# Optimization experiments

Measured on AMD Instinct MI355X. Metric: run time of the kernel, lower is better.

Reference implementation:

```python
import jax, jax.numpy as jnp
import numpy as np

B, TQ, TK, QD, KD = 16, 256, 256, 512, 512

def setup_inputs() -> dict:
    key = jax.random.key(0)
    k = jax.random.split(key, 8)
    query = jax.random.normal(k[0], (B, TQ, QD), dtype=jnp.float32)
    keys = jax.random.normal(k[1], (B, TK, KD), dtype=jnp.float32)
    # linear_q: query_size -> key_size (stored as [in, out] for x @ W)
    Wq = jax.random.normal(k[2], (QD, KD), dtype=jnp.float32) * 0.02
    bq = jnp.zeros((KD,), dtype=jnp.float32)
    # linear_att: key_size -> 1
    w_att = jax.random.normal(k[3], (KD,), dtype=jnp.float32) * 0.02
    b_att = jnp.zeros((), dtype=jnp.float32)
    # linear_out: (query_size + key_size) -> query_size
    Wout = jax.random.normal(k[4], (QD + KD, QD), dtype=jnp.float32) * 0.02
    bout = jnp.zeros((QD,), dtype=jnp.float32)
    return {"query": query, "keys": keys, "Wq": Wq, "bq": bq,
            "w_att": w_att, "b_att": b_att, "Wout": Wout, "bout": bout}

def reference(query, keys, Wq, bq, w_att, b_att, Wout, bout):
    # att_query = linear_q(query): [b, t_q, n]
    att_query = query @ Wq + bq
    # Bahdanau additive score: tanh(q_i + k_j) . w + b  -> [b, t_q, t_k]
    sum_qk = jnp.tanh(att_query[:, :, None, :] + keys[:, None, :, :])  # b,tq,tk,n
    scores = jnp.einsum('bqkn,n->bqk', sum_qk, w_att) + b_att
    p = jax.nn.softmax(scores, axis=-1)  # softmax over t_k
    # values defaults to keys
    context = jnp.einsum('bqk,bkn->bqn', p, keys)
    # output transform: tanh(linear_out([query; context]))
    context = jnp.tanh(jnp.concatenate([query, context], axis=-1) @ Wout + bout)
    return context, p
```

## Files before the change

### kernel.cpp

```cpp
#include <hip/hip_runtime.h>


#define C2 2.88539008177792681f

typedef unsigned short u16;
typedef short s16x8 __attribute__((ext_vector_type(8)));
typedef float f32x4 __attribute__((ext_vector_type(4)));

__device__ __forceinline__ float fast_rcp(float x) { return __builtin_amdgcn_rcpf(x); }

__device__ __forceinline__ u16 f2bf(float f) {
  union { float f; unsigned u; } v; v.f = f;
  unsigned r = v.u + 0x7fffu + ((v.u >> 16) & 1u);
  return (u16)(r >> 16);
}
__device__ __forceinline__ unsigned packbf(float a, float b) {
  return (unsigned)f2bf(a) | ((unsigned)f2bf(b) << 16);
}

__global__ __launch_bounds__(256) void prep_kernel(
    const float* __restrict__ keys, float* __restrict__ Ek,
    const float* __restrict__ query, u16* __restrict__ qbf,
    const float* __restrict__ w_att, const float* __restrict__ b_att,
    float* __restrict__ Cout)
{
  __shared__ float red[4];
  const int t = threadIdx.x;
  const int bx = blockIdx.x;
  if (bx < 2048) {
    const size_t i4 = (size_t)bx * 256 + t;
    float4 v = ((const float4*)keys)[i4];
    float4 o;
    o.x = exp2f(C2 * v.x); o.y = exp2f(C2 * v.y);
    o.z = exp2f(C2 * v.z); o.w = exp2f(C2 * v.w);
    ((float4*)Ek)[i4] = o;
    if (bx == 0) {
      float wsum = w_att[t] + w_att[t + 256];
#pragma unroll
      for (int m = 32; m; m >>= 1) wsum += __shfl_xor(wsum, m);
      if ((t & 63) == 0) red[t >> 6] = wsum;
      __syncthreads();
      if (t == 0) Cout[0] = red[0] + red[1] + red[2] + red[3] + b_att[0];
    }
  } else {
    const size_t i8 = ((size_t)(bx - 2048) * 256 + t) * 8;
    float4 a = *(const float4*)&query[i8];
    float4 b = *(const float4*)&query[i8 + 4];
    unsigned p0 = packbf(a.x, a.y), p1 = packbf(a.z, a.w);
    unsigned p2 = packbf(b.x, b.y), p3 = packbf(b.z, b.w);
    *(int4*)&qbf[i8] = make_int4(p0, p1, p2, p3);
  }
}

__global__ __launch_bounds__(256) void transpose_w_bf16(
    const float* __restrict__ Wq, u16* __restrict__ Wqt,
    const float* __restrict__ Wout, u16* __restrict__ Woutt)
{
  __shared__ u16 tile[32][40];
  const int t = threadIdx.x;
  const int by = blockIdx.y;
  const float* W; u16* Wt; int K, k0;
  if (by < 16) { W = Wq;   Wt = Wqt;   K = 512;  k0 = by * 32; }
  else         { W = Wout; Wt = Woutt; K = 1024; k0 = (by - 16) * 32; }
  const int n0 = blockIdx.x * 32;
  const int r = t >> 3, c = (t & 7) * 4;
  float4 v = *(const float4*)&W[(size_t)(k0 + r) * 512 + n0 + c];
  tile[c + 0][r] = f2bf(v.x); tile[c + 1][r] = f2bf(v.y);
  tile[c + 2][r] = f2bf(v.z); tile[c + 3][r] = f2bf(v.w);
  __syncthreads();
  if (t < 128) {
    const int row = t >> 2, ch = (t & 3) * 8;
    unsigned p0 = (unsigned)tile[row][ch + 0] | ((unsigned)tile[row][ch + 1] << 16);
    unsigned p1 = (unsigned)tile[row][ch + 2] | ((unsigned)tile[row][ch + 3] << 16);
    unsigned p2 = (unsigned)tile[row][ch + 4] | ((unsigned)tile[row][ch + 5] << 16);
    unsigned p3 = (unsigned)tile[row][ch + 6] | ((unsigned)tile[row][ch + 7] << 16);
    *(int4*)&Wt[(size_t)(n0 + row) * K + k0 + ch] = make_int4(p0, p1, p2, p3);
  }
}

__global__ __launch_bounds__(256) void transpose_keys_bf16(
    const float* __restrict__ keys, u16* __restrict__ kbfT)
{
  __shared__ u16 tile[32][40];
  const int t = threadIdx.x;
  const int n0 = blockIdx.x * 32, k0 = blockIdx.y * 32, b = blockIdx.z;
  const float* src = keys + (size_t)b * 131072;
  u16* dst = kbfT + (size_t)b * 131072;
  const int r = t >> 3, c = (t & 7) * 4;
  float4 v = *(const float4*)&src[(size_t)(k0 + r) * 512 + n0 + c];
  tile[c + 0][r] = f2bf(v.x); tile[c + 1][r] = f2bf(v.y);
  tile[c + 2][r] = f2bf(v.z); tile[c + 3][r] = f2bf(v.w);
  __syncthreads();
  if (t < 128) {
    const int row = t >> 2, ch = (t & 3) * 8;
    unsigned p0 = (unsigned)tile[row][ch + 0] | ((unsigned)tile[row][ch + 1] << 16);
    unsigned p1 = (unsigned)tile[row][ch + 2] | ((unsigned)tile[row][ch + 3] << 16);
    unsigned p2 = (unsigned)tile[row][ch + 4] | ((unsigned)tile[row][ch + 5] << 16);
    unsigned p3 = (unsigned)tile[row][ch + 6] | ((unsigned)tile[row][ch + 7] << 16);
    *(int4*)&dst[(size_t)(n0 + row) * 256 + k0 + ch] = make_int4(p0, p1, p2, p3);
  }
}

__global__ __launch_bounds__(256) void gemm_mfma_bf16(
    const u16* __restrict__ A0, const u16* __restrict__ A1, int kSplit,
    const u16* __restrict__ Bt, const float* __restrict__ bias,
    float* __restrict__ C, int K, int act)
{
  __shared__ u16 As[64 * 72];
  __shared__ u16 Bs[64 * 72];
  const int t = threadIdx.x;
  const int lane = t & 63, wid = t >> 6;
  const int wm = wid >> 1, wn = wid & 1;
  const int col0 = blockIdx.x * 64, row0 = blockIdx.y * 64;
  const int lr = t >> 2, lc = (t & 3) * 16;
  const int fr = lane & 15, fg = (lane >> 4) * 8;

  f32x4 acc[2][2] = {};
  const int nIter = K >> 6;

  int4 a0v, a1v, b0v, b1v;
  {
    const u16* Asrc = (0 < kSplit) ? A0 : A1;
    a0v = *(const int4*)&Asrc[(size_t)(row0 + lr) * 512 + lc];
    a1v = *(const int4*)&Asrc[(size_t)(row0 + lr) * 512 + lc + 8];
    b0v = *(const int4*)&Bt[(size_t)(col0 + lr) * K + lc];
    b1v = *(const int4*)&Bt[(size_t)(col0 + lr) * K + lc + 8];
  }
  for (int it = 0; it < nIter; ++it) {
    __syncthreads();
    *(int4*)&As[lr * 72 + lc]     = a0v;
    *(int4*)&As[lr * 72 + lc + 8] = a1v;
    *(int4*)&Bs[lr * 72 + lc]     = b0v;
    *(int4*)&Bs[lr * 72 + lc + 8] = b1v;
    __syncthreads();

    if (it + 1 < nIter) {
      const int k0 = (it + 1) << 6;
      const u16* Asrc; int kc;
      if (k0 < kSplit) { Asrc = A0; kc = k0; } else { Asrc = A1; kc = k0 - kSplit; }
      a0v = *(const int4*)&Asrc[(size_t)(row0 + lr) * 512 + kc + lc];
      a1v = *(const int4*)&Asrc[(size_t)(row0 + lr) * 512 + kc + lc + 8];
      b0v = *(const int4*)&Bt[(size_t)(col0 + lr) * K + k0 + lc];
      b1v = *(const int4*)&Bt[(size_t)(col0 + lr) * K + k0 + lc + 8];
    }

#pragma unroll
    for (int ks = 0; ks < 2; ++ks) {
      s16x8 af[2], bf[2];
#pragma unroll
      for (int m = 0; m < 2; ++m)
        af[m] = *(const s16x8*)&As[(wm * 32 + m * 16 + fr) * 72 + ks * 32 + fg];
#pragma unroll
      for (int n = 0; n < 2; ++n)
        bf[n] = *(const s16x8*)&Bs[(wn * 32 + n * 16 + fr) * 72 + ks * 32 + fg];
#pragma unroll
      for (int m = 0; m < 2; ++m)
#pragma unroll
        for (int n = 0; n < 2; ++n)
          acc[m][n] = __builtin_amdgcn_mfma_f32_16x16x32_bf16(af[m], bf[n], acc[m][n], 0, 0, 0);
    }
  }

  const int fq = lane >> 4;
#pragma unroll
  for (int n = 0; n < 2; ++n) {
    const int col = col0 + wn * 32 + n * 16 + fr;
    const float bv = bias[col];
#pragma unroll
    for (int m = 0; m < 2; ++m) {
#pragma unroll
      for (int i = 0; i < 4; ++i) {
        const int row = row0 + wm * 32 + m * 16 + fq * 4 + i;
        float v = acc[m][n][i] + bv;
        if (act == 1) {
          float e = __expf(2.0f * v);
          v = 1.0f - 2.0f * fast_rcp(e + 1.0f);
        } else if (act == 2) {
          v = exp2f(C2 * v);
        }
        C[(size_t)row * 512 + col] = v;
      }
    }
  }
}

__global__ __launch_bounds__(256) void score_kernel(
    const float* __restrict__ Ea, const float* __restrict__ Ek,
    const float* __restrict__ w_att, const float* __restrict__ Cptr,
    float* __restrict__ S)
{
  __shared__ float ea_s[64][68];
  __shared__ float ek_s[64][68];
  __shared__ float w_s[128];

  const int z = blockIdx.z;
  const int b = z >> 2, qt = z & 3;
  const int q0 = blockIdx.y * 64, k0 = blockIdx.x * 64;
  const int t = threadIdx.x;
  if (t < 128) w_s[t] = w_att[qt * 128 + t];

  const int qi = t >> 4, ki = t & 15;
  const int lr = t >> 2, lc = (t & 3) * 16;
  const float* eap = Ea + (size_t)(b * 256 + q0) * 512 + qt * 128;
  const float* ekp = Ek + (size_t)(b * 256 + k0) * 512 + qt * 128;

  float acc[4][4] = {};

  for (int c = 0; c < 2; ++c) {
    const int gb = lr * 512 + c * 64 + lc;
    float4 A0 = *(const float4*)&eap[gb + 0];
    float4 A1 = *(const float4*)&eap[gb + 4];
    float4 A2 = *(const float4*)&eap[gb + 8];
    float4 A3 = *(const float4*)&eap[gb + 12];
    float4 K0 = *(const float4*)&ekp[gb + 0];
    float4 K1 = *(const float4*)&ekp[gb + 4];
    float4 K2 = *(const float4*)&ekp[gb + 8];
    float4 K3 = *(const float4*)&ekp[gb + 12];
    __syncthreads();
    *(float4*)&ea_s[lr][lc + 0]  = A0;
    *(float4*)&ea_s[lr][lc + 4]  = A1;
    *(float4*)&ea_s[lr][lc + 8]  = A2;
    *(float4*)&ea_s[lr][lc + 12] = A3;
    *(float4*)&ek_s[lr][lc + 0]  = K0;
    *(float4*)&ek_s[lr][lc + 4]  = K1;
    *(float4*)&ek_s[lr][lc + 8]  = K2;
    *(float4*)&ek_s[lr][lc + 12] = K3;
    __syncthreads();

    for (int j = 0; j < 64; j += 4) {
      float4 av[4], kv[4];
#pragma unroll
      for (int m = 0; m < 4; ++m) av[m] = *(const float4*)&ea_s[qi + m * 16][j];
#pragma unroll
      for (int n = 0; n < 4; ++n) kv[n] = *(const float4*)&ek_s[ki + n * 16][j];
      float4 wv = *(const float4*)&w_s[c * 64 + j];
#pragma unroll
      for (int m = 0; m < 4; ++m) {
#pragma unroll
        for (int n = 0; n < 4; ++n) {
          float q1 = fmaf(av[m].x, kv[n].x, 1.0f);
          float q2 = fmaf(av[m].y, kv[n].y, 1.0f);
          float q3 = fmaf(av[m].z, kv[n].z, 1.0f);
          float q4 = fmaf(av[m].w, kv[n].w, 1.0f);
          float N12 = fmaf(wv.x, q2, wv.y * q1);
          float D12 = q1 * q2;
          float N34 = fmaf(wv.z, q4, wv.w * q3);
          float D34 = q3 * q4;
          float Nt = fmaf(N12, D34, N34 * D12);
          float Dt = D12 * D34;
          acc[m][n] = fmaf(Nt, fast_rcp(Dt), acc[m][n]);
        }
      }
    }
  }

  const float Cv = (qt == 0) ? Cptr[0] : 0.0f;
  float* sc = S + (size_t)qt * 1048576;
#pragma unroll
  for (int m = 0; m < 4; ++m) {
    const size_t qr = (size_t)(b * 256 + q0 + qi + m * 16);
#pragma unroll
    for (int n = 0; n < 4; ++n)
      sc[qr * 256 + k0 + ki + n * 16] = fmaf(-2.f, acc[m][n], Cv);
  }
}

__global__ __launch_bounds__(256) void softmax_kernel(
    const float* __restrict__ S, float* __restrict__ p_out,
    u16* __restrict__ pbf)
{
  const int t = threadIdx.x;
  const int w = t >> 6, lane = t & 63;
  const int row = blockIdx.x * 4 + w;
  const size_t off = (size_t)row * 256 + lane * 4;
  float4 sa = *(const float4*)&S[off];
  float4 sb = *(const float4*)&S[off + 1048576];
  float4 sc = *(const float4*)&S[off + 2097152];
  float4 sd = *(const float4*)&S[off + 3145728];
  float4 s4 = {(sa.x + sb.x) + (sc.x + sd.x), (sa.y + sb.y) + (sc.y + sd.y),
               (sa.z + sb.z) + (sc.z + sd.z), (sa.w + sb.w) + (sc.w + sd.w)};
  float m = fmaxf(fmaxf(s4.x, s4.y), fmaxf(s4.z, s4.w));
#pragma unroll
  for (int msk = 32; msk; msk >>= 1) m = fmaxf(m, __shfl_xor(m, msk));
  float e0 = __expf(s4.x - m);
  float e1 = __expf(s4.y - m);
  float e2 = __expf(s4.z - m);
  float e3 = __expf(s4.w - m);
  float ssum = (e0 + e1) + (e2 + e3);
#pragma unroll
  for (int msk = 32; msk; msk >>= 1) ssum += __shfl_xor(ssum, msk);
  float rs = 1.0f / ssum;
  float4 p4 = {e0 * rs, e1 * rs, e2 * rs, e3 * rs};
  *(float4*)&p_out[off] = p4;
  unsigned lo = packbf(p4.x, p4.y), hi = packbf(p4.z, p4.w);
  *(int2*)&pbf[off] = make_int2(lo, hi);
}

__global__ __launch_bounds__(256) void ctx_gemm(
    const u16* __restrict__ pbf, const u16* __restrict__ kbfT,
    u16* __restrict__ ctxbf)
{
  __shared__ u16 As[64 * 72];
  __shared__ u16 Bs[64 * 72];
  const int t = threadIdx.x;
  const int lane = t & 63, wid = t >> 6;
  const int wm = wid >> 1, wn = wid & 1;
  const int col0 = blockIdx.x * 64, row0 = blockIdx.y * 64, b = blockIdx.z;
  const u16* A = pbf + (size_t)b * 65536;
  const u16* Bm = kbfT + (size_t)b * 131072;
  const int lr = t >> 2, lc = (t & 3) * 16;
  const int fr = lane & 15, fg = (lane >> 4) * 8;

  f32x4 acc[2][2] = {};

  int4 a0v = *(const int4*)&A[(size_t)(row0 + lr) * 256 + lc];
  int4 a1v = *(const int4*)&A[(size_t)(row0 + lr) * 256 + lc + 8];
  int4 b0v = *(const int4*)&Bm[(size_t)(col0 + lr) * 256 + lc];
  int4 b1v = *(const int4*)&Bm[(size_t)(col0 + lr) * 256 + lc + 8];

  for (int it = 0; it < 4; ++it) {
    __syncthreads();
    *(int4*)&As[lr * 72 + lc]     = a0v;
    *(int4*)&As[lr * 72 + lc + 8] = a1v;
    *(int4*)&Bs[lr * 72 + lc]     = b0v;
    *(int4*)&Bs[lr * 72 + lc + 8] = b1v;
    __syncthreads();

    if (it < 3) {
      const int k0 = (it + 1) << 6;
      a0v = *(const int4*)&A[(size_t)(row0 + lr) * 256 + k0 + lc];
      a1v = *(const int4*)&A[(size_t)(row0 + lr) * 256 + k0 + lc + 8];
      b0v = *(const int4*)&Bm[(size_t)(col0 + lr) * 256 + k0 + lc];
      b1v = *(const int4*)&Bm[(size_t)(col0 + lr) * 256 + k0 + lc + 8];
    }

#pragma unroll
    for (int ks = 0; ks < 2; ++ks) {
      s16x8 af[2], bf[2];
#pragma unroll
      for (int m = 0; m < 2; ++m)
        af[m] = *(const s16x8*)&As[(wm * 32 + m * 16 + fr) * 72 + ks * 32 + fg];
#pragma unroll
      for (int n = 0; n < 2; ++n)
        bf[n] = *(const s16x8*)&Bs[(wn * 32 + n * 16 + fr) * 72 + ks * 32 + fg];
#pragma unroll
      for (int m = 0; m < 2; ++m)
#pragma unroll
        for (int n = 0; n < 2; ++n)
          acc[m][n] = __builtin_amdgcn_mfma_f32_16x16x32_bf16(af[m], bf[n], acc[m][n], 0, 0, 0);
    }
  }

  const int fq = lane >> 4;
#pragma unroll
  for (int n = 0; n < 2; ++n) {
    const int col = col0 + wn * 32 + n * 16 + fr;
#pragma unroll
    for (int m = 0; m < 2; ++m) {
#pragma unroll
      for (int i = 0; i < 4; ++i) {
        const int row = row0 + wm * 32 + m * 16 + fq * 4 + i;
        ctxbf[(size_t)(b * 256 + row) * 512 + col] = f2bf(acc[m][n][i]);
      }
    }
  }
}

extern "C" void kernel_launch(void* const* d_in, const int* in_sizes, int n_in,
                              void* d_out, int out_size, void* d_ws, size_t ws_size,
                              hipStream_t stream) {
  const float* query = (const float*)d_in[0];
  const float* keys  = (const float*)d_in[1];
  const float* Wq    = (const float*)d_in[2];
  const float* bq    = (const float*)d_in[3];
  const float* w_att = (const float*)d_in[4];
  const float* b_att = (const float*)d_in[5];
  const float* Wout  = (const float*)d_in[6];
  const float* bout  = (const float*)d_in[7];

  float* out_tanh = (float*)d_out;
  float* out_p    = out_tanh + (size_t)4096 * 512;

  float* ws = (float*)d_ws;
  float* Ea     = ws;
  float* Ek     = ws + 2097152;
  float* S      = ws + 4194304;
  float* Cptr   = ws + 8388608;
  u16*   Wqt    = (u16*)(ws + 8388624);
  u16*   Woutt  = Wqt + 262144;
  u16*   qbf    = Woutt + 524288;
  u16*   ctxbf  = (u16*)Ea;
  u16*   kbfT   = (u16*)Ek;
  u16*   pbf    = kbfT + 2097152;

  prep_kernel<<<3072, 256, 0, stream>>>(keys, Ek, query, qbf, w_att, b_att, Cptr);
  transpose_w_bf16<<<dim3(16, 48), 256, 0, stream>>>(Wq, Wqt, Wout, Woutt);

  gemm_mfma_bf16<<<dim3(8, 64), 256, 0, stream>>>(
      qbf, qbf, 512, Wqt, bq, Ea, 512, 2);

  score_kernel<<<dim3(4, 4, 64), 256, 0, stream>>>(
      Ea, Ek, w_att, Cptr, S);

  transpose_keys_bf16<<<dim3(16, 8, 16), 256, 0, stream>>>(keys, kbfT);

  softmax_kernel<<<1024, 256, 0, stream>>>(S, out_p, pbf);

  ctx_gemm<<<dim3(8, 4, 16), 256, 0, stream>>>(pbf, kbfT, ctxbf);

  gemm_mfma_bf16<<<dim3(8, 64), 256, 0, stream>>>(
      qbf, ctxbf, 512, Woutt, bout, out_tanh, 1024, 1);
}
```

Baseline: 102.6 us.

## Merge prep kernels into one launch and pack score math into float2 FMAs

Folds the key exp, query bf16 cast, key transpose and weight transposes into a single mega_prep launch, cutting two kernel launches. kbfT moves to its own workspace slot instead of aliasing Ek, so the transpose can run before the score kernel. The score kernel's inner loop now works on f32x2 vectors to allow packed FMA/mul instructions on MI355X, and reads w_att from global memory instead of shared memory. The costs are more register pressure and uniform global loads for w_att inside the hot loop.

```diff
diff --git a/kernel.cpp b/kernel.cpp
--- a/kernel.cpp
+++ b/kernel.cpp
@@ -6,8 +6,12 @@
 typedef unsigned short u16;
 typedef short s16x8 __attribute__((ext_vector_type(8)));
 typedef float f32x4 __attribute__((ext_vector_type(4)));
+typedef float f32x2 __attribute__((ext_vector_type(2)));
 
 __device__ __forceinline__ float fast_rcp(float x) { return __builtin_amdgcn_rcpf(x); }
+__device__ __forceinline__ f32x2 fma2(f32x2 a, f32x2 b, f32x2 c) {
+  return __builtin_elementwise_fma(a, b, c);
+}
 
 __device__ __forceinline__ u16 f2bf(float f) {
   union { float f; unsigned u; } v; v.f = f;
@@ -18,15 +22,20 @@
   return (unsigned)f2bf(a) | ((unsigned)f2bf(b) << 16);
 }
 
-__global__ __launch_bounds__(256) void prep_kernel(
+__global__ __launch_bounds__(256) void mega_prep(
     const float* __restrict__ keys, float* __restrict__ Ek,
     const float* __restrict__ query, u16* __restrict__ qbf,
+    u16* __restrict__ kbfT,
+    const float* __restrict__ Wq, u16* __restrict__ Wqt,
+    const float* __restrict__ Wout, u16* __restrict__ Woutt,
     const float* __restrict__ w_att, const float* __restrict__ b_att,
-    float* __restrict__ Cout)
+    float* __restrict__ Cptr)
 {
   __shared__ float red[4];
+  __shared__ u16 tile[32][40];
   const int t = threadIdx.x;
   const int bx = blockIdx.x;
+
   if (bx < 2048) {
     const size_t i4 = (size_t)bx * 256 + t;
     float4 v = ((const float4*)keys)[i4];
@@ -40,64 +49,53 @@
       for (int m = 32; m; m >>= 1) wsum += __shfl_xor(wsum, m);
       if ((t & 63) == 0) red[t >> 6] = wsum;
       __syncthreads();
-      if (t == 0) Cout[0] = red[0] + red[1] + red[2] + red[3] + b_att[0];
-    }
-  } else {
+      if (t == 0) Cptr[0] = red[0] + red[1] + red[2] + red[3] + b_att[0];
+    }
+  } else if (bx < 3072) {
     const size_t i8 = ((size_t)(bx - 2048) * 256 + t) * 8;
     float4 a = *(const float4*)&query[i8];
     float4 b = *(const float4*)&query[i8 + 4];
     unsigned p0 = packbf(a.x, a.y), p1 = packbf(a.z, a.w);
     unsigned p2 = packbf(b.x, b.y), p3 = packbf(b.z, b.w);
     *(int4*)&qbf[i8] = make_int4(p0, p1, p2, p3);
-  }
-}
-
-__global__ __launch_bounds__(256) void transpose_w_bf16(
-    const float* __restrict__ Wq, u16* __restrict__ Wqt,
-    const float* __restrict__ Wout, u16* __restrict__ Woutt)
-{
-  __shared__ u16 tile[32][40];
-  const int t = threadIdx.x;
-  const int by = blockIdx.y;
-  const float* W; u16* Wt; int K, k0;
-  if (by < 16) { W = Wq;   Wt = Wqt;   K = 512;  k0 = by * 32; }
-  else         { W = Wout; Wt = Woutt; K = 1024; k0 = (by - 16) * 32; }
-  const int n0 = blockIdx.x * 32;
-  const int r = t >> 3, c = (t & 7) * 4;
-  float4 v = *(const float4*)&W[(size_t)(k0 + r) * 512 + n0 + c];
-  tile[c + 0][r] = f2bf(v.x); tile[c + 1][r] = f2bf(v.y);
-  tile[c + 2][r] = f2bf(v.z); tile[c + 3][r] = f2bf(v.w);
-  __syncthreads();
-  if (t < 128) {
-    const int row = t >> 2, ch = (t & 3) * 8;
-    unsigned p0 = (unsigned)tile[row][ch + 0] | ((unsigned)tile[row][ch + 1] << 16);
-    unsigned p1 = (unsigned)tile[row][ch + 2] | ((unsigned)tile[row][ch + 3] << 16);
-    unsigned p2 = (unsigned)tile[row][ch + 4] | ((unsigned)tile[row][ch + 5] << 16);
-    unsigned p3 = (unsigned)tile[row][ch + 6] | ((unsigned)tile[row][ch + 7] << 16);
-    *(int4*)&Wt[(size_t)(n0 + row) * K + k0 + ch] = make_int4(p0, p1, p2, p3);
-  }
-}
-
-__global__ __launch_bounds__(256) void transpose_keys_bf16(
-    const float* __restrict__ keys, u16* __restrict__ kbfT)
-{
-  __shared__ u16 tile[32][40];
-  const int t = threadIdx.x;
-  const int n0 = blockIdx.x * 32, k0 = blockIdx.y * 32, b = blockIdx.z;
-  const float* src = keys + (size_t)b * 131072;
-  u16* dst = kbfT + (size_t)b * 131072;
-  const int r = t >> 3, c = (t & 7) * 4;
-  float4 v = *(const float4*)&src[(size_t)(k0 + r) * 512 + n0 + c];
-  tile[c + 0][r] = f2bf(v.x); tile[c + 1][r] = f2bf(v.y);
-  tile[c + 2][r] = f2bf(v.z); tile[c + 3][r] = f2bf(v.w);
-  __syncthreads();
-  if (t < 128) {
-    const int row = t >> 2, ch = (t & 3) * 8;
-    unsigned p0 = (unsigned)tile[row][ch + 0] | ((unsigned)tile[row][ch + 1] << 16);
-    unsigned p1 = (unsigned)tile[row][ch + 2] | ((unsigned)tile[row][ch + 3] << 16);
-    unsigned p2 = (unsigned)tile[row][ch + 4] | ((unsigned)tile[row][ch + 5] << 16);
-    unsigned p3 = (unsigned)tile[row][ch + 6] | ((unsigned)tile[row][ch + 7] << 16);
-    *(int4*)&dst[(size_t)(n0 + row) * 256 + k0 + ch] = make_int4(p0, p1, p2, p3);
+  } else if (bx < 5120) {
+    const int b2 = bx - 3072;
+    const int n0 = (b2 & 15) * 32, k0 = ((b2 >> 4) & 7) * 32, b = b2 >> 7;
+    const float* src = keys + (size_t)b * 131072;
+    u16* dst = kbfT + (size_t)b * 131072;
+    const int r = t >> 3, c = (t & 7) * 4;
+    float4 v = *(const float4*)&src[(size_t)(k0 + r) * 512 + n0 + c];
+    tile[c + 0][r] = f2bf(v.x); tile[c + 1][r] = f2bf(v.y);
+    tile[c + 2][r] = f2bf(v.z); tile[c + 3][r] = f2bf(v.w);
+    __syncthreads();
+    if (t < 128) {
+      const int row = t >> 2, ch = (t & 3) * 8;
+      unsigned p0 = (unsigned)tile[row][ch + 0] | ((unsigned)tile[row][ch + 1] << 16);
+      unsigned p1 = (unsigned)tile[row][ch + 2] | ((unsigned)tile[row][ch + 3] << 16);
+      unsigned p2 = (unsigned)tile[row][ch + 4] | ((unsigned)tile[row][ch + 5] << 16);
+      unsigned p3 = (unsigned)tile[row][ch + 6] | ((unsigned)tile[row][ch + 7] << 16);
+      *(int4*)&dst[(size_t)(n0 + row) * 256 + k0 + ch] = make_int4(p0, p1, p2, p3);
+    }
+  } else {
+    const int b3 = bx - 5120;
+    const int by = b3 >> 4;
+    const int n0 = (b3 & 15) * 32;
+    const float* W; u16* Wt; int K, k0;
+    if (by < 16) { W = Wq;   Wt = Wqt;   K = 512;  k0 = by * 32; }
+    else         { W = Wout; Wt = Woutt; K = 1024; k0 = (by - 16) * 32; }
+    const int r = t >> 3, c = (t & 7) * 4;
+    float4 v = *(const float4*)&W[(size_t)(k0 + r) * 512 + n0 + c];
+    tile[c + 0][r] = f2bf(v.x); tile[c + 1][r] = f2bf(v.y);
+    tile[c + 2][r] = f2bf(v.z); tile[c + 3][r] = f2bf(v.w);
+    __syncthreads();
+    if (t < 128) {
+      const int row = t >> 2, ch = (t & 3) * 8;
+      unsigned p0 = (unsigned)tile[row][ch + 0] | ((unsigned)tile[row][ch + 1] << 16);
+      unsigned p1 = (unsigned)tile[row][ch + 2] | ((unsigned)tile[row][ch + 3] << 16);
+      unsigned p2 = (unsigned)tile[row][ch + 4] | ((unsigned)tile[row][ch + 5] << 16);
+      unsigned p3 = (unsigned)tile[row][ch + 6] | ((unsigned)tile[row][ch + 7] << 16);
+      *(int4*)&Wt[(size_t)(n0 + row) * K + k0 + ch] = make_int4(p0, p1, p2, p3);
+    }
   }
 }
 
@@ -191,20 +189,20 @@
 {
   __shared__ float ea_s[64][68];
   __shared__ float ek_s[64][68];
-  __shared__ float w_s[128];
 
   const int z = blockIdx.z;
   const int b = z >> 2, qt = z & 3;
   const int q0 = blockIdx.y * 64, k0 = blockIdx.x * 64;
   const int t = threadIdx.x;
-  if (t < 128) w_s[t] = w_att[qt * 128 + t];
 
   const int qi = t >> 4, ki = t & 15;
   const int lr = t >> 2, lc = (t & 3) * 16;
   const float* eap = Ea + (size_t)(b * 256 + q0) * 512 + qt * 128;
   const float* ekp = Ek + (size_t)(b * 256 + k0) * 512 + qt * 128;
+  const float* wbase = w_att + qt * 128;
 
   float acc[4][4] = {};
+  const f32x2 one = {1.0f, 1.0f};
 
   for (int c = 0; c < 2; ++c) {
     const int gb = lr * 512 + c * 64 + lc;
@@ -227,28 +225,47 @@
     *(float4*)&ek_s[lr][lc + 12] = K3;
     __syncthreads();
 
-    for (int j = 0; j < 64; j += 4) {
-      float4 av[4], kv[4];
-#pragma unroll
-      for (int m = 0; m < 4; ++m) av[m] = *(const float4*)&ea_s[qi + m * 16][j];
-#pragma unroll
-      for (int n = 0; n < 4; ++n) kv[n] = *(const float4*)&ek_s[ki + n * 16][j];
-      float4 wv = *(const float4*)&w_s[c * 64 + j];
+    for (int j = 0; j < 64; j += 8) {
+      f32x2 kp[4][4];
+#pragma unroll
+      for (int n = 0; n < 4; ++n) {
+        float4 kv0 = *(const float4*)&ek_s[ki + n * 16][j];
+        float4 kv1 = *(const float4*)&ek_s[ki + n * 16][j + 4];
+        kp[n][0] = f32x2{kv0.x, kv0.y};
+        kp[n][1] = f32x2{kv0.z, kv0.w};
+        kp[n][2] = f32x2{kv1.x, kv1.y};
+        kp[n][3] = f32x2{kv1.z, kv1.w};
+      }
+      const float* wq = wbase + c * 64 + j;
+      f32x2 wp0 = {wq[0], wq[1]};
+      f32x2 wp1 = {wq[2], wq[3]};
+      f32x2 wp2 = {wq[4], wq[5]};
+      f32x2 wp3 = {wq[6], wq[7]};
+
 #pragma unroll
       for (int m = 0; m < 4; ++m) {
+        float4 av0 = *(const float4*)&ea_s[qi + m * 16][j];
+        float4 av1 = *(const float4*)&ea_s[qi + m * 16][j + 4];
+        f32x2 ap0 = {av0.x, av0.y};
+        f32x2 ap1 = {av0.z, av0.w};
+        f32x2 ap2 = {av1.x, av1.y};
+        f32x2 ap3 = {av1.z, av1.w};
 #pragma unroll
         for (int n = 0; n < 4; ++n) {
-          float q1 = fmaf(av[m].x, kv[n].x, 1.0f);
-          float q2 = fmaf(av[m].y, kv[n].y, 1.0f);
-          float q3 = fmaf(av[m].z, kv[n].z, 1.0f);
-          float q4 = fmaf(av[m].w, kv[n].w, 1.0f);
-          float N12 = fmaf(wv.x, q2, wv.y * q1);
-          float D12 = q1 * q2;
-          float N34 = fmaf(wv.z, q4, wv.w * q3);
-          float D34 = q3 * q4;
-          float Nt = fmaf(N12, D34, N34 * D12);
-          float Dt = D12 * D34;
-          acc[m][n] = fmaf(Nt, fast_rcp(Dt), acc[m][n]);
+          f32x2 q1 = fma2(ap0, kp[n][0], one);
+          f32x2 q2 = fma2(ap1, kp[n][1], one);
+          f32x2 q3 = fma2(ap2, kp[n][2], one);
+          f32x2 q4 = fma2(ap3, kp[n][3], one);
+          f32x2 N12 = fma2(wp0, q2, wp1 * q1);
+          f32x2 D12 = q1 * q2;
+          f32x2 N34 = fma2(wp2, q4, wp3 * q3);
+          f32x2 D34 = q3 * q4;
+          f32x2 Nt = fma2(N12, D34, N34 * D12);
+          f32x2 Dt = D12 * D34;
+          float r0 = fast_rcp(Dt.x);
+          float r1 = fast_rcp(Dt.y);
+          acc[m][n] = fmaf(Nt.x, r0, acc[m][n]);
+          acc[m][n] = fmaf(Nt.y, r1, acc[m][n]);
         }
       }
     }
@@ -389,12 +406,12 @@
   u16*   Wqt    = (u16*)(ws + 8388624);
   u16*   Woutt  = Wqt + 262144;
   u16*   qbf    = Woutt + 524288;
+  u16*   kbfT   = qbf + 2097152;
+  u16*   pbf    = kbfT + 2097152;
   u16*   ctxbf  = (u16*)Ea;
-  u16*   kbfT   = (u16*)Ek;
-  u16*   pbf    = kbfT + 2097152;
-
-  prep_kernel<<<3072, 256, 0, stream>>>(keys, Ek, query, qbf, w_att, b_att, Cptr);
-  transpose_w_bf16<<<dim3(16, 48), 256, 0, stream>>>(Wq, Wqt, Wout, Woutt);
+
+  mega_prep<<<5888, 256, 0, stream>>>(
+      keys, Ek, query, qbf, kbfT, Wq, Wqt, Wout, Woutt, w_att, b_att, Cptr);
 
   gemm_mfma_bf16<<<dim3(8, 64), 256, 0, stream>>>(
       qbf, qbf, 512, Wqt, bq, Ea, 512, 2);
@@ -402,8 +419,6 @@
   score_kernel<<<dim3(4, 4, 64), 256, 0, stream>>>(
       Ea, Ek, w_att, Cptr, S);
 
-  transpose_keys_bf16<<<dim3(16, 8, 16), 256, 0, stream>>>(keys, kbfT);
-
   softmax_kernel<<<1024, 256, 0, stream>>>(S, out_p, pbf);
 
   ctx_gemm<<<dim3(8, 4, 16), 256, 0, stream>>>(pbf, kbfT, ctxbf);
```

Measured after the change: 101.0 us. No clear change (-1.5%).
